# Performance work log

Hardware: AMD Instinct MI355X
Metric: run time of the kernel (lower is better)

The kernel has to match this reference:

```python
import jax, jax.numpy as jnp
import numpy as np

SUB, E_NO, I_NO = 20, 2000, 500
T_DATA, T_SYN, T_HIST = 20000, 200, 50
SB, HB = 3, 3


def setup_inputs() -> dict:
    key = jax.random.key(0)
    ks = jax.random.split(key, 14)
    S_e = (jax.random.uniform(ks[0], (T_DATA, E_NO)) < 0.02).astype(jnp.float32)
    S_i = (jax.random.uniform(ks[1], (T_DATA, I_NO)) < 0.02).astype(jnp.float32)
    C_den = (jax.random.uniform(ks[2], (SUB, SUB)) < 0.1).astype(jnp.float32)
    C_syn_e = (jax.random.uniform(ks[3], (SUB, E_NO)) < 0.05).astype(jnp.float32)
    C_syn_i = (jax.random.uniform(ks[4], (SUB, I_NO)) < 0.05).astype(jnp.float32)
    W_syn = 0.1 * jax.random.normal(ks[5], (SUB, SB, 2))
    Tau_syn = jnp.tile(jnp.arange(SB, dtype=jnp.float32)[:, None], (1, 2))
    Delta_syn = jax.random.uniform(ks[6], (SUB, 2))
    W_hist = 0.1 * jax.random.normal(ks[7], (SUB, HB))
    Tau_hist = jnp.arange(HB, dtype=jnp.float32)
    Delta_hist = jax.random.uniform(ks[8], (SUB,))
    W_sub = jax.random.uniform(ks[9], (SUB,))
    V_o = jax.random.normal(ks[10], (1,))
    Theta = jnp.zeros((SUB,), jnp.float32)
    return {"S_e": S_e, "S_i": S_i, "C_den": C_den, "C_syn_e": C_syn_e,
            "C_syn_i": C_syn_i, "W_syn": W_syn, "Tau_syn": Tau_syn,
            "Delta_syn": Delta_syn, "W_hist": W_hist, "Tau_hist": Tau_hist,
            "Delta_hist": Delta_hist, "W_sub": W_sub, "V_o": V_o, "Theta": Theta}


def _alpha_kernels(delta, tau_log, W, T):
    # delta: [sub], tau_log: [B], W: [sub, B] -> kernels [sub, T]
    t = jnp.maximum(jnp.arange(T, dtype=jnp.float32)[None, :] - delta[:, None], 0.0)  # [sub,T]
    tt = t[:, None, :] / jnp.exp(tau_log)[None, :, None]  # [sub,B,T]
    return jnp.einsum('sbt,sb->st', tt * jnp.exp(-tt), W)


def _causal_conv(x, kern):
    # x: [T, sub], kern: [sub, T_k]; out[t,s] = sum_k kern[s,k] * x[t-k,s]
    Tk = kern.shape[1]
    xp = jnp.pad(x.T[None], ((0, 0), (0, 0), (Tk - 1, 0)))  # [1, sub, T+Tk-1]
    out = jax.lax.conv_general_dilated(
        xp, jnp.flip(kern, 1)[:, None, :], (1,), 'VALID',
        feature_group_count=kern.shape[0])
    return out[0].T  # [T, sub]


def reference(S_e, S_i, C_den, C_syn_e, C_syn_i, W_syn, Tau_syn, Delta_syn,
              W_hist, Tau_hist, Delta_hist, W_sub, V_o, Theta):
    # --- synaptic drive (vectorized over subunits) ---
    ke = _alpha_kernels(jnp.exp(Delta_syn[:, 0]), Tau_syn[:, 0], W_syn[:, :, 0], T_SYN)
    ki = _alpha_kernels(jnp.exp(Delta_syn[:, 1]), Tau_syn[:, 1], W_syn[:, :, 1], T_SYN)
    in_e = S_e @ C_syn_e.T  # [T, sub]
    in_i = S_i @ C_syn_i.T
    syn_in = _causal_conv(in_e, ke) + _causal_conv(in_i, ki)  # [T, sub]

    # --- history kernel ---
    hist_kern = _alpha_kernels(Delta_hist, Tau_hist, W_hist, T_HIST)  # [sub, T_hist]
    K = jnp.flip(hist_kern, 1)  # K[s, j] multiplies buffer entry j (oldest first)

    # --- sequential recurrence via scan ---
    def step(buf, syn_t):
        # buf: [T_hist, sub] = Y_pad[t : t+T_hist]
        h = jnp.einsum('js,sj->s', buf, K)
        prop = (buf[-1] * W_sub) @ C_den.T
        y = jnp.tanh(syn_t + prop + Theta + h)
        buf = jnp.concatenate([buf[1:], y[None]], 0)
        return buf, y

    buf0 = jnp.zeros((T_HIST, SUB), syn_in.dtype)
    _, Y = jax.lax.scan(step, buf0, syn_in)  # Y: [T, sub]
    return Y[:, 0] * W_sub[0] + V_o[0]
```

## Files before the change

### kernel.cpp

```cpp
#include <hip/hip_runtime.h>
#include <hip/hip_bf16.h>
#include <stdint.h>
#include <type_traits>

#define SUBU 20
#define E_NO 2000
#define I_NO 500
#define T_DATA 20000
#define T_SYNK 200
#define HBAS 3
#define SBAS 3
#define TPAD 20096

#define OFF_SYN  0
#define OFF_INE  401920
#define OFF_INI  803840
#define OFF_KE   1205760
#define OFF_KI   1209760
#define OFF_IIR  1213760
#define OFF_MW   1214760
#define OFF_MIDX 1215000
#define OFF_PAR  1215240
#define OFF_FLAG 1215264
#define OFF_Y    OFF_INI
#define KSTORE   12

#define TKC 2.8853900817779268f

__device__ __forceinline__ float bf2f(unsigned short u){
  unsigned v = ((unsigned)u) << 16; float f; __builtin_memcpy(&f, &v, 4); return f;
}
__device__ __forceinline__ float ldany(const void* p, int i, int bf){
  return bf ? bf2f(((const unsigned short*)p)[i]) : ((const float*)p)[i];
}
__device__ __forceinline__ float ex2(float x){ return __builtin_amdgcn_exp2f(x); }
__device__ __forceinline__ float rcpa(float x){ return __builtin_amdgcn_rcpf(x); }

__global__ __launch_bounds__(512) void k_prep(
    const void* Se, const void* Cden, const void* Wsyn, const void* Tausyn,
    const void* Dsyn, const void* Whist, const void* Tauhist, const void* Dhist,
    const void* Wsub, const void* Vo, const void* Theta, float* ws){
  int* wsi = (int*)ws;
  const int tx = threadIdx.x;
  __shared__ int found, mx;
  if (tx == 0){ found = 0; mx = 0; }
  __syncthreads();
  {
    const unsigned* w = (const unsigned*)Se;
    int hit = 0;
    for (int i = tx; i < 8192; i += 512){
      unsigned x = w[i];
      if (x == 0x00003F80u || x == 0x3F803F80u) hit = 1;
    }
    if (hit) atomicOr(&found, 1);
  }
  __syncthreads();
  const int bf = found;
  if (tx == 0) wsi[OFF_FLAG] = bf;
  for (int idx = tx; idx < SUBU * T_SYNK; idx += 512){
    int s = idx / T_SYNK, t = idx % T_SYNK;
    for (int c = 0; c < 2; ++c){
      float delta = __expf(ldany(Dsyn, s*2 + c, bf));
      float acc = 0.f;
      for (int b = 0; b < SBAS; ++b){
        float tau = __expf(ldany(Tausyn, b*2 + c, bf));
        float w   = ldany(Wsyn, (s*SBAS + b)*2 + c, bf);
        float tt  = fmaxf((float)t - delta, 0.f) / tau;
        acc += w * tt * __expf(-tt);
      }
      ws[(c == 0 ? OFF_KE : OFF_KI) + s*T_SYNK + t] = acc;
    }
  }
  if (tx < SUBU * HBAS){
    int s = tx / HBAS, b = tx % HBAS;
    float tau = __expf(ldany(Tauhist, b, bf));
    float w   = TKC * ldany(Whist, s*HBAS + b, bf);
    float dl  = ldany(Dhist, s, bf);
    float rho = __expf(-1.f / tau);
    float e1  = __expf(-(1.f - dl) / tau);
    float g1  = ((1.f - dl) / tau) * e1;
    float kap = rho / tau;
    float* c = ws + OFF_IIR + s*16 + b*4;
    c[0] = rho;
    c[1] = w * kap;
    c[2] = w * g1;
    c[3] = e1;
    if (b == 2){
      float e49 = __expf(-(49.f - dl) / tau);
      float g49 = ((49.f - dl) / tau) * e49;
      ws[OFF_IIR + s*16 + 12] = w * (rho*g49 + kap*e49);
      ws[OFF_IIR + s*16 + 13] = rho * e49;
    }
  }
  if (tx < SUBU){
    int s = tx, cnt = 0;
    float rowsum = 0.f;
    for (int sp = 0; sp < SUBU; ++sp){
      float c = ldany(Cden, s*SUBU + sp, bf);
      if (c != 0.f && cnt < KSTORE){
        float m = c * ldany(Wsub, sp, bf);
        rowsum += m;
        ws[OFF_MW + s*KSTORE + cnt]  = -2.f * TKC * m;
        wsi[OFF_MIDX + s*KSTORE + cnt] = sp;
        ++cnt;
      }
    }
    for (int k = cnt; k < KSTORE; ++k){
      ws[OFF_MW + s*KSTORE + k] = 0.f; wsi[OFF_MIDX + s*KSTORE + k] = 0;
    }
    atomicMax(&mx, cnt);
    ws[OFF_PAR + s] = TKC * (ldany(Theta, s, bf) + rowsum);
  }
  __syncthreads();
  if (tx == 0){
    ws[OFF_PAR + SUBU]     = ldany(Wsub, 0, bf);
    ws[OFF_PAR + SUBU + 1] = ldany(Vo, 0, bf);
    wsi[OFF_PAR + 23] = (mx <= 3) ? 3 : (mx <= 4 ? 4 : (mx <= 5 ? 5 :
                        (mx <= 6 ? 6 : 12)));
  }
}

template<int BF>
__device__ __forceinline__ void gemm_impl(const void* S, const void* C, int W,
                                          float* dst, int t0, int lane){
  float acc[4][SUBU];
  #pragma unroll
  for (int r = 0; r < 4; ++r)
    #pragma unroll
    for (int s = 0; s < SUBU; ++s) acc[r][s] = 0.f;
  for (int e = lane; e < W; e += 64){
    float s0 = ldany(S, (t0+0)*W + e, BF);
    float s1 = ldany(S, (t0+1)*W + e, BF);
    float s2 = ldany(S, (t0+2)*W + e, BF);
    float s3 = ldany(S, (t0+3)*W + e, BF);
    #pragma unroll
    for (int s = 0; s < SUBU; ++s){
      float c = ldany(C, s*W + e, BF);
      acc[0][s] = fmaf(s0, c, acc[0][s]);
      acc[1][s] = fmaf(s1, c, acc[1][s]);
      acc[2][s] = fmaf(s2, c, acc[2][s]);
      acc[3][s] = fmaf(s3, c, acc[3][s]);
    }
  }
  #pragma unroll
  for (int r = 0; r < 4; ++r){
    #pragma unroll
    for (int s = 0; s < SUBU; ++s){
      float v = acc[r][s];
      #pragma unroll
      for (int m = 32; m >= 1; m >>= 1) v += __shfl_xor(v, m, 64);
      if (lane == 0) dst[s*TPAD + t0 + r] = v;
    }
  }
}

__global__ __launch_bounds__(256) void k_gemm(const void* S, const void* C, int W,
                                              float* dst, const int* flagp){
  const int wave = threadIdx.x >> 6, lane = threadIdx.x & 63;
  const int t0 = blockIdx.x * 16 + wave * 4;
  if (*flagp) gemm_impl<1>(S, C, W, dst, t0, lane);
  else        gemm_impl<0>(S, C, W, dst, t0, lane);
}

__global__ __launch_bounds__(256) void k_conv(float* ws){
  const int s  = blockIdx.y;
  const int t0 = blockIdx.x * 256;
  const float* ine = ws + OFF_INE + s*TPAD;
  const float* ini = ws + OFF_INI + s*TPAD;
  __shared__ float eL[455], iL[455], keL[T_SYNK], kiL[T_SYNK];
  for (int j = threadIdx.x; j < 455; j += 256){
    int t = t0 - 199 + j;
    bool ok = (t >= 0 && t < TPAD);
    eL[j] = ok ? ine[t] : 0.f;
    iL[j] = ok ? ini[t] : 0.f;
  }
  for (int j = threadIdx.x; j < T_SYNK; j += 256){
    keL[j] = ws[OFF_KE + s*T_SYNK + j];
    kiL[j] = ws[OFF_KI + s*T_SYNK + j];
  }
  __syncthreads();
  int t = t0 + threadIdx.x;
  if (t < TPAD){
    float a0 = 0.f, a1 = 0.f;
    #pragma unroll 4
    for (int k = 0; k < T_SYNK; ++k){
      a0 = fmaf(keL[k], eL[threadIdx.x + 199 - k], a0);
      a1 = fmaf(kiL[k], iL[threadIdx.x + 199 - k], a1);
    }
    ws[OFF_SYN + s*TPAD + t] = fmaf(TKC, a0 + a1, ws[OFF_PAR + s]);
  }
}

__device__ __forceinline__ float get4(const float4& a, const float4& b,
                                      const float4& c, const float4& d, int u){
  const float4& q = (u < 4) ? a : ((u < 8) ? b : ((u < 12) ? c : d));
  int r = u & 3;
  return (r == 0) ? q.x : ((r == 1) ? q.y : ((r == 2) ? q.z : q.w));
}
__device__ __forceinline__ void set4(float4& a, float4& b, float4& c, float4& d,
                                     int u, float v){
  float4& q = (u < 4) ? a : ((u < 8) ? b : ((u < 12) ? c : d));
  int r = u & 3;
  if (r == 0) q.x = v; else if (r == 1) q.y = v; else if (r == 2) q.z = v; else q.w = v;
}

template<int KM>
__global__ __launch_bounds__(64, 1) void k_scan(float* ws, float* yout){
  const int* wsi = (const int*)ws;
  if (wsi[OFF_PAR + 23] != KM) return;
  __shared__ float ring[64*68];
  const int lane = threadIdx.x;
  const int s = lane < SUBU ? lane : SUBU - 1;
  float* rbase = &ring[lane*68];
  {
    float4 z = make_float4(0.f, 0.f, 0.f, 0.f);
    float4* rq = (float4*)rbase;
    #pragma unroll
    for (int j = 0; j < 16; ++j) rq[j] = z;
  }
  float mwp[KM]; int mad[KM];
  #pragma unroll
  for (int k = 0; k < KM; ++k){
    mwp[k] = ws[OFF_MW + s*KSTORE + k];
    mad[k] = wsi[OFF_MIDX + s*KSTORE + k] * 4;
  }
  const float* cc = ws + OFF_IIR + s*16;
  const float rh0 = cc[0],  kp0 = cc[1],  ay0 = cc[2],  ey0 = cc[3];
  const float rh1 = cc[4],  kp1 = cc[5],  ay1 = cc[6],  ey1 = cc[7];
  const float rh2 = cc[8],  kp2 = cc[9],  ay2 = cc[10], ey2 = cc[11];
  const float cA  = cc[12], cE  = cc[13];
  const float wsub0 = ws[OFF_PAR + SUBU];
  const float vo    = ws[OFF_PAR + SUBU + 1];
  const float* syncol = ws + OFF_SYN + s*TPAD;

  float A0=0.f,E0=0.f,A1=0.f,E1=0.f,A2=0.f,E2=0.f;
  float pb[KM];
  #pragma unroll
  for (int k = 0; k < KM; ++k) pb[k] = 0.5f;
  float yprev = 0.f;
  float roN   = 0.f;
  float4 u0 = *(const float4*)(syncol + 0);
  float4 u1 = *(const float4*)(syncol + 4);
  float4 u2 = *(const float4*)(syncol + 8);
  float4 u3 = *(const float4*)(syncol + 12);
  float4 n0, n1, n2, n3;
  float xpre = u0.x;

  auto block16 = [&](auto PH_, int tbase, float4& b0, float4& b1, float4& b2,
                     float4& b3, float4& p0, float4& p1, float4& p2, float4& p3){
    constexpr int PH = decltype(PH_)::value;
    const float4* src = (const float4*)(syncol + tbase + 16);
    p0 = src[0]; p1 = src[1]; p2 = src[2]; p3 = src[3];
    float4 ob0, ob1, ob2, ob3;
    #pragma unroll
    for (int u = 0; u < 16; ++u){
      float acc0 = fmaf(mwp[0], pb[0], xpre);
      float acc1 = mwp[1] * pb[1];
      #pragma unroll
      for (int k = 2; k < KM; ++k){
        if (k & 1) acc1 = fmaf(mwp[k], pb[k], acc1);
        else       acc0 = fmaf(mwp[k], pb[k], acc0);
      }
      float X  = acc0 + acc1;
      float r  = rcpa(ex2(X) + 1.f);
      int rb = __float_as_int(r);
      #pragma unroll
      for (int k = 0; k < KM; ++k)
        pb[k] = __int_as_float(__builtin_amdgcn_ds_bpermute(mad[k], rb));
      float y = fmaf(-2.f, r, 1.f);
      float ro = roN;
      float A0n = fmaf(rh0, A0, fmaf(kp0, E0, ay0 * yprev));
      E0 = fmaf(rh0, E0, ey0 * yprev); A0 = A0n;
      float A1n = fmaf(rh1, A1, fmaf(kp1, E1, ay1 * yprev));
      E1 = fmaf(rh1, E1, ey1 * yprev); A1 = A1n;
      float A2n = fmaf(rh2, A2, fmaf(kp2, E2, fmaf(-cA, ro, ay2 * yprev)));
      E2 = fmaf(rh2, E2, fmaf(-cE, ro, ey2 * yprev)); A2 = A2n;
      float h = (A0 + A1) + A2;
      float cn = (u < 15) ? get4(b0, b1, b2, b3, u + 1) : p0.x;
      xpre = cn + h;
      rbase[PH + u] = y;
      roN = rbase[(PH + u + 15) & 63];
      yprev = y;
      set4(ob0, ob1, ob2, ob3, u, fmaf(y, wsub0, vo));
    }
    if (lane == 0 && tbase + 16 <= T_DATA){
      float4* q = (float4*)(yout + tbase);
      q[0] = ob0; q[1] = ob1; q[2] = ob2; q[3] = ob3;
    }
  };

  using P0  = std::integral_constant<int,0>;
  using P16 = std::integral_constant<int,16>;
  using P32 = std::integral_constant<int,32>;
  using P48 = std::integral_constant<int,48>;
  #pragma unroll 1
  for (int ib2 = 0; ib2 < 314; ++ib2){
    const int tb = ib2 * 64;
    block16(P0{},  tb,      u0, u1, u2, u3, n0, n1, n2, n3);
    block16(P16{}, tb + 16, n0, n1, n2, n3, u0, u1, u2, u3);
    block16(P32{}, tb + 32, u0, u1, u2, u3, n0, n1, n2, n3);
    block16(P48{}, tb + 48, n0, n1, n2, n3, u0, u1, u2, u3);
  }
}

__global__ __launch_bounds__(256) void k_out(const float* ws, void* outp){
  const int* wsi = (const int*)ws;
  const int bf = wsi[OFF_FLAG];
  int i = blockIdx.x * 256 + threadIdx.x;
  if (i < T_DATA){
    float v = ws[OFF_Y + i];
    if (bf) ((__hip_bfloat16*)outp)[i] = __float2bfloat16(v);
    else    ((float*)outp)[i] = v;
  }
}

extern "C" void kernel_launch(void* const* d_in, const int* in_sizes, int n_in,
                              void* d_out, int out_size, void* d_ws, size_t ws_size,
                              hipStream_t stream){
  const void* S_e   = d_in[0];
  const void* S_i   = d_in[1];
  const void* C_den = d_in[2];
  const void* C_e   = d_in[3];
  const void* C_i   = d_in[4];
  const void* W_syn = d_in[5];
  const void* Tau_s = d_in[6];
  const void* D_syn = d_in[7];
  const void* W_hst = d_in[8];
  const void* Tau_h = d_in[9];
  const void* D_hst = d_in[10];
  const void* W_sub = d_in[11];
  const void* V_o   = d_in[12];
  const void* Theta = d_in[13];
  float* ws = (float*)d_ws;
  int* flagp = (int*)(ws + OFF_FLAG);

  k_prep<<<1, 512, 0, stream>>>(S_e, C_den, W_syn, Tau_s, D_syn, W_hst, Tau_h,
                                D_hst, W_sub, V_o, Theta, ws);
  k_gemm<<<1250, 256, 0, stream>>>(S_e, C_e, E_NO, ws + OFF_INE, flagp);
  k_gemm<<<1250, 256, 0, stream>>>(S_i, C_i, I_NO, ws + OFF_INI, flagp);
  dim3 cgrid(79, 20);
  k_conv<<<cgrid, 256, 0, stream>>>(ws);
  float* yout = ws + OFF_Y;
  k_scan<3><<<1, 64, 0, stream>>>(ws, yout);
  k_scan<4><<<1, 64, 0, stream>>>(ws, yout);
  k_scan<5><<<1, 64, 0, stream>>>(ws, yout);
  k_scan<6><<<1, 64, 0, stream>>>(ws, yout);
  k_scan<12><<<1, 64, 0, stream>>>(ws, yout);
  k_out<<<79, 256, 0, stream>>>(ws, d_out);
}
```

Measured before the change: 1.995 ms.

## Merge scan variants into one launch, batch ring-buffer I/O, write output directly

Replaces five template-specialized scan launches (four of which exit early) and the separate output-conversion kernel with a single scan kernel that switches on the fan-in count at runtime and writes fp32 or bf16 output directly. The per-step shared-memory ring store and load of the delayed history value is replaced by one vector load of 16 old values before each 16-step block and paired float2 stores after it. This removes per-step LDS latency from the serial dependency chain and saves five kernel launches. It adds a runtime switch and larger code, and the batched ring layout must stay consistent with the 15-step delay offset.

```diff
diff --git a/kernel.cpp b/kernel.cpp
--- a/kernel.cpp
+++ b/kernel.cpp
@@ -1,6 +1,7 @@
 #include <hip/hip_runtime.h>
 #include <hip/hip_bf16.h>
 #include <stdint.h>
+#include <string.h>
 #include <type_traits>
 
 #define SUBU 20
@@ -22,7 +23,6 @@
 #define OFF_MIDX 1215000
 #define OFF_PAR  1215240
 #define OFF_FLAG 1215264
-#define OFF_Y    OFF_INI
 #define KSTORE   12
 
 #define TKC 2.8853900817779268f
@@ -205,11 +205,8 @@
 }
 
 template<int KM>
-__global__ __launch_bounds__(64, 1) void k_scan(float* ws, float* yout){
+__device__ void scan_body(float* ws, void* outp, int bf, int lane, float* ring){
   const int* wsi = (const int*)ws;
-  if (wsi[OFF_PAR + 23] != KM) return;
-  __shared__ float ring[64*68];
-  const int lane = threadIdx.x;
   const int s = lane < SUBU ? lane : SUBU - 1;
   float* rbase = &ring[lane*68];
   {
@@ -238,7 +235,6 @@
   #pragma unroll
   for (int k = 0; k < KM; ++k) pb[k] = 0.5f;
   float yprev = 0.f;
-  float roN   = 0.f;
   float4 u0 = *(const float4*)(syncol + 0);
   float4 u1 = *(const float4*)(syncol + 4);
   float4 u2 = *(const float4*)(syncol + 8);
@@ -251,11 +247,15 @@
     constexpr int PH = decltype(PH_)::value;
     const float4* src = (const float4*)(syncol + tbase + 16);
     p0 = src[0]; p1 = src[1]; p2 = src[2]; p3 = src[3];
+    constexpr int RO = (PH + 16) & 63;
+    const float4* rr = (const float4*)(rbase + RO);
+    float4 yo0 = rr[0], yo1 = rr[1], yo2 = rr[2], yo3 = rr[3];
     float4 ob0, ob1, ob2, ob3;
+    float4 yb0, yb1, yb2, yb3;
     #pragma unroll
     for (int u = 0; u < 16; ++u){
       float acc0 = fmaf(mwp[0], pb[0], xpre);
-      float acc1 = mwp[1] * pb[1];
+      float acc1 = (KM > 1) ? mwp[1] * pb[1] : 0.f;
       #pragma unroll
       for (int k = 2; k < KM; ++k){
         if (k & 1) acc1 = fmaf(mwp[k], pb[k], acc1);
@@ -268,7 +268,7 @@
       for (int k = 0; k < KM; ++k)
         pb[k] = __int_as_float(__builtin_amdgcn_ds_bpermute(mad[k], rb));
       float y = fmaf(-2.f, r, 1.f);
-      float ro = roN;
+      float ro = get4(yo0, yo1, yo2, yo3, u);
       float A0n = fmaf(rh0, A0, fmaf(kp0, E0, ay0 * yprev));
       E0 = fmaf(rh0, E0, ey0 * yprev); A0 = A0n;
       float A1n = fmaf(rh1, A1, fmaf(kp1, E1, ay1 * yprev));
@@ -278,14 +278,37 @@
       float h = (A0 + A1) + A2;
       float cn = (u < 15) ? get4(b0, b1, b2, b3, u + 1) : p0.x;
       xpre = cn + h;
-      rbase[PH + u] = y;
-      roN = rbase[(PH + u + 15) & 63];
       yprev = y;
+      set4(yb0, yb1, yb2, yb3, u, y);
       set4(ob0, ob1, ob2, ob3, u, fmaf(y, wsub0, vo));
     }
+    #pragma unroll
+    for (int i = 0; i < 8; ++i){
+      constexpr_hint:
+      ;
+      int pos = (PH + 2 + 2*i) & 63;
+      *(float2*)(rbase + pos) =
+        make_float2(get4(yb0, yb1, yb2, yb3, 2*i),
+                    get4(yb0, yb1, yb2, yb3, 2*i + 1));
+    }
     if (lane == 0 && tbase + 16 <= T_DATA){
-      float4* q = (float4*)(yout + tbase);
-      q[0] = ob0; q[1] = ob1; q[2] = ob2; q[3] = ob3;
+      if (bf){
+        unsigned w[8];
+        #pragma unroll
+        for (int i = 0; i < 8; ++i){
+          __hip_bfloat16 lo = __float2bfloat16(get4(ob0, ob1, ob2, ob3, 2*i));
+          __hip_bfloat16 hi = __float2bfloat16(get4(ob0, ob1, ob2, ob3, 2*i + 1));
+          unsigned short ulo, uhi;
+          __builtin_memcpy(&ulo, &lo, 2); __builtin_memcpy(&uhi, &hi, 2);
+          w[i] = (unsigned)ulo | ((unsigned)uhi << 16);
+        }
+        uint4* q = (uint4*)((__hip_bfloat16*)outp + tbase);
+        q[0] = make_uint4(w[0], w[1], w[2], w[3]);
+        q[1] = make_uint4(w[4], w[5], w[6], w[7]);
+      } else {
+        float4* q = (float4*)((float*)outp + tbase);
+        q[0] = ob0; q[1] = ob1; q[2] = ob2; q[3] = ob3;
+      }
     }
   };
 
@@ -303,14 +326,18 @@
   }
 }
 
-__global__ __launch_bounds__(256) void k_out(const float* ws, void* outp){
+__global__ __launch_bounds__(64, 1) void k_scan(float* ws, void* outp){
+  __shared__ float ring[64*68];
   const int* wsi = (const int*)ws;
-  const int bf = wsi[OFF_FLAG];
-  int i = blockIdx.x * 256 + threadIdx.x;
-  if (i < T_DATA){
-    float v = ws[OFF_Y + i];
-    if (bf) ((__hip_bfloat16*)outp)[i] = __float2bfloat16(v);
-    else    ((float*)outp)[i] = v;
+  const int bf   = wsi[OFF_FLAG];
+  const int ksel = wsi[OFF_PAR + 23];
+  const int lane = threadIdx.x;
+  switch (ksel){
+    case 3:  scan_body<3>(ws, outp, bf, lane, ring); break;
+    case 4:  scan_body<4>(ws, outp, bf, lane, ring); break;
+    case 5:  scan_body<5>(ws, outp, bf, lane, ring); break;
+    case 6:  scan_body<6>(ws, outp, bf, lane, ring); break;
+    default: scan_body<12>(ws, outp, bf, lane, ring); break;
   }
 }
 
@@ -340,11 +367,5 @@
   k_gemm<<<1250, 256, 0, stream>>>(S_i, C_i, I_NO, ws + OFF_INI, flagp);
   dim3 cgrid(79, 20);
   k_conv<<<cgrid, 256, 0, stream>>>(ws);
-  float* yout = ws + OFF_Y;
-  k_scan<3><<<1, 64, 0, stream>>>(ws, yout);
-  k_scan<4><<<1, 64, 0, stream>>>(ws, yout);
-  k_scan<5><<<1, 64, 0, stream>>>(ws, yout);
-  k_scan<6><<<1, 64, 0, stream>>>(ws, yout);
-  k_scan<12><<<1, 64, 0, stream>>>(ws, yout);
-  k_out<<<79, 256, 0, stream>>>(ws, d_out);
-}
+  k_scan<<<1, 64, 0, stream>>>(ws, d_out);
+}
```

Measured after the change: 1.963 ms. About the same (-1.6%).
